# Kernel tuning notes

Measured on AMD Instinct MI355X. Metric: run time of the kernel, lower is better.

Reference implementation:

```python
import jax, jax.numpy as jnp
import numpy as np

N = 50000      # nodes
E = 800000     # edges (avg degree 16)
D = 128        # embed_dim
H = 8          # nhead
HD = D // H    # head dim = 16


def setup_inputs() -> dict:
    key = jax.random.key(0)
    ks = jax.random.split(key, 6)
    s = 1.0 / np.sqrt(D)  # ~xavier scale for square matrices
    return {
        "feats": jax.random.normal(ks[0], (N, D), jnp.float32),
        "edge_index": jax.random.randint(ks[1], (E, 2), 0, N, dtype=jnp.int64),
        "Wq": jax.random.normal(ks[2], (D, D), jnp.float32) * s,
        "bq": jnp.zeros((D,), jnp.float32),
        "Wk": jax.random.normal(ks[3], (D, D), jnp.float32) * s,
        "bk": jnp.zeros((D,), jnp.float32),
        "Wv": jax.random.normal(ks[4], (D, D), jnp.float32) * s,
        "bv": jnp.zeros((D,), jnp.float32),
        "Wo": jax.random.normal(ks[5], (D, D), jnp.float32) * s,
        "bo": jnp.zeros((D,), jnp.float32),
    }


def reference(feats, edge_index, Wq, bq, Wk, bk, Wv, bv, Wo, bo):
    # Projections (nn.Linear: x @ W.T + b), split into heads: [N, H, HD]
    q = (feats @ Wq.T + bq).reshape(N, H, HD)
    k = (feats @ Wk.T + bk).reshape(N, H, HD)
    v = (feats @ Wv.T + bv).reshape(N, H, HD)

    r = edge_index[:, 0]  # source nodes
    c = edge_index[:, 1]  # destination nodes (softmax / aggregation groups)

    # Per-edge, per-head dot-product scores: [E, H]
    scores = jnp.einsum('ehd,ehd->eh', q[c], k[r]) / np.sqrt(HD)

    # Custom scatter-softmax: src_max clamped to min 0; extra exp(-src_max) in denom
    smax = jnp.maximum(jax.ops.segment_max(scores, c, num_segments=N), 0.0)  # [N, H]
    ex = jnp.exp(scores - smax[c])                                           # [E, H]
    denom = jax.ops.segment_sum(ex, c, num_segments=N)                       # [N, H]
    attn = ex / (denom + jnp.exp(-smax))[c]                                  # [E, H]

    # Weighted V per edge, scatter-mean to destination nodes
    out_e = attn[:, :, None] * v[r]                      # [E, H, HD]
    agg = jax.ops.segment_sum(out_e, c, num_segments=N)  # [N, H, HD]
    cnt = jax.ops.segment_sum(jnp.ones((E,), jnp.float32), c, num_segments=N)
    agg = agg / jnp.maximum(cnt, 1.0)[:, None, None]

    return agg.reshape(N, D) @ Wo.T + bo
```

## Files before the change

### kernel.cpp

```cpp
#include <hip/hip_runtime.h>
#include <hip/hip_bf16.h>

#define N_NODES 50000
#define N_EDGES 800000
#define DIM 128
#define NHEAD 8
#define HDIM 16
#define ELL_PAD 64
#define ELL_SLICES 391
#define ELL_BLOCKS (8 * ELL_SLICES)
#define ROWTILES 3125
#define OUT_WAVES (ROWTILES * 2)
#define OUT_GRID ((OUT_WAVES + 3) / 4)

#define Q_OFF      0ull
#define KV_OFF     12800000ull
#define AGG_OFF    38400000ull
#define ELL_OFF    51200000ull
#define CNT_OFF    64000000ull
#define WBF_OFF    64200192ull
#define BIAS_OFF   64331264ull

typedef __attribute__((ext_vector_type(8))) short short8;
typedef __attribute__((ext_vector_type(4))) float floatx4;

__device__ inline float bflo2f(unsigned u) { return __uint_as_float(u << 16); }
__device__ inline float bfhi2f(unsigned u) { return __uint_as_float(u & 0xffff0000u); }
__device__ inline unsigned short f2bf(float f) {
    unsigned u = __float_as_uint(f);
    return (unsigned short)((u + 0x7fffu + ((u >> 16) & 1u)) >> 16);
}

__device__ inline void detect_flags(const void* feats, const void* edge,
                                    int& isbf, int& is32) {
    const unsigned short* f = (const unsigned short*)feats;
    const unsigned int* eg = (const unsigned int*)edge;
    int lane = threadIdx.x & 63;
    unsigned e = (f[lane] >> 7) & 0xFF;
    int junk = (e >= 0x90 || (e > 0 && e <= 0x60)) ? 1 : 0;
    unsigned long long jm = __ballot(junk);
    int nz = (lane < 32 && eg[2 * lane + 1] != 0) ? 1 : 0;
    unsigned long long nm = __ballot(nz);
    isbf = (jm == 0ull) ? 1 : 0;
    is32 = (nm != 0ull) ? 1 : 0;
}

__device__ inline void load_edge(const int* edge, int is32, int e, int& r, int& c) {
    if (is32) { int2 p = ((const int2*)edge)[e]; r = p.x; c = p.y; }
    else {
        const long long* p = (const long long*)edge;
        r = (int)p[2 * e]; c = (int)p[2 * e + 1];
    }
    if ((unsigned)r >= N_NODES) r = 0;
    if ((unsigned)c >= N_NODES) c = 0;
}

__device__ inline float ldf(const void* p, int isbf, int i) {
    return isbf ? __bfloat162float(((const __hip_bfloat16*)p)[i])
                : ((const float*)p)[i];
}

__device__ inline short8 ldfrag(const void* base, int isbf, size_t off) {
    if (isbf) return *(const short8*)((const unsigned short*)base + off);
    const float* f = (const float*)base + off;
    float4 f0 = *(const float4*)f;
    float4 f1 = *(const float4*)(f + 4);
    short8 a;
    a[0] = (short)f2bf(f0.x); a[1] = (short)f2bf(f0.y);
    a[2] = (short)f2bf(f0.z); a[3] = (short)f2bf(f0.w);
    a[4] = (short)f2bf(f1.x); a[5] = (short)f2bf(f1.y);
    a[6] = (short)f2bf(f1.z); a[7] = (short)f2bf(f1.w);
    return a;
}

__global__ __launch_bounds__(256) void ell_build(const void* feats, const int* edge,
                                                 const void* wq, const void* wk,
                                                 const void* wv, const void* wo,
                                                 const void* bq, const void* bk,
                                                 const void* bv, const void* bo,
                                                 int* cnt, int* ell,
                                                 unsigned short* wbf, float* bias) {
    int isbf, is32; detect_flags(feats, edge, isbf, is32);

    if (blockIdx.x >= ELL_BLOCKS) {
        int b2 = blockIdx.x - ELL_BLOCKS;
        if (b2 == 256) {
            for (int j = threadIdx.x; j < 512; j += 256) {
                int m2 = j >> 7;
                const void* bb = (m2 == 0) ? bq : (m2 == 1) ? bk : (m2 == 2) ? bv : bo;
                bias[j] = ldf(bb, isbf, j & 127);
            }
            return;
        }
        if (isbf) return;
        int idx = b2 * 256 + (int)threadIdx.x;
        int mm = idx >> 14, rem = idx & 16383;
        const void* wsrc = (mm == 0) ? wq : (mm == 1) ? wk : (mm == 2) ? wv : wo;
        wbf[idx] = f2bf(((const float*)wsrc)[rem]);
        return;
    }

    int pid = blockIdx.x & 7, slice = blockIdx.x >> 3;
    int base = slice * 2048 + (int)threadIdx.x;
    #pragma unroll
    for (int j = 0; j < 8; ++j) {
        int e = base + j * 256;
        if (e < N_EDGES) {
            int r, c; load_edge(edge, is32, e, r, c);
            if ((c & 7) == pid) {
                int slot = atomicAdd(cnt + c, 1);
                if (slot < ELL_PAD) ell[c * ELL_PAD + slot] = r;
            }
        }
    }
}

__global__ __launch_bounds__(192) void qkv_mfma(const void* feats_raw, const int* edge,
                                                const void* wq_raw, const void* wk_raw,
                                                const void* wv_raw,
                                                const unsigned short* wbf,
                                                const float* bias,
                                                unsigned short* q_s, unsigned short* kv_s) {
    int isbf, is32; detect_flags(feats_raw, edge, isbf, is32);
    int rowtile = blockIdx.x;
    int m = threadIdx.x >> 6;
    int lane = threadIdx.x & 63;
    int mrow = lane & 15, quad = lane >> 4;
    int arow = rowtile * 16 + mrow;

    short8 a[4];
    #pragma unroll
    for (int kt = 0; kt < 4; ++kt)
        a[kt] = ldfrag(feats_raw, isbf, (size_t)arow * DIM + quad * 8 + kt * 32);

    const void* wraw = (m == 0) ? wq_raw : (m == 1) ? wk_raw : wv_raw;
    const unsigned short* wm = isbf ? (const unsigned short*)wraw : wbf + m * 16384;
    int soff = (m == 2) ? 16 : 0;

    for (int nt = 0; nt < 8; ++nt) {
        float b = bias[m * 128 + nt * 16 + mrow];
        floatx4 acc = {b, b, b, b};
        const unsigned short* wp = wm + (size_t)(nt * 16 + mrow) * DIM + quad * 8;
        #pragma unroll
        for (int kt = 0; kt < 4; ++kt) {
            short8 bf = *(const short8*)(wp + kt * 32);
            acc = __builtin_amdgcn_mfma_f32_16x16x32_bf16(a[kt], bf, acc, 0, 0, 0);
        }
        if (m == 0) {
            #pragma unroll
            for (int r4 = 0; r4 < 4; ++r4) {
                int row = rowtile * 16 + quad * 4 + r4;
                q_s[(size_t)row * DIM + nt * 16 + mrow] = f2bf(acc[r4]);
            }
        } else {
            #pragma unroll
            for (int r4 = 0; r4 < 4; ++r4) {
                int row = rowtile * 16 + quad * 4 + r4;
                kv_s[(size_t)row * 256 + nt * 32 + soff + mrow] = f2bf(acc[r4]);
            }
        }
    }
}

__device__ __forceinline__ float dot16(uint4 ka, uint4 kb, const float* qv) {
    float s = 0.f;
    s += bflo2f(ka.x) * qv[0]  + bfhi2f(ka.x) * qv[1];
    s += bflo2f(ka.y) * qv[2]  + bfhi2f(ka.y) * qv[3];
    s += bflo2f(ka.z) * qv[4]  + bfhi2f(ka.z) * qv[5];
    s += bflo2f(ka.w) * qv[6]  + bfhi2f(ka.w) * qv[7];
    s += bflo2f(kb.x) * qv[8]  + bfhi2f(kb.x) * qv[9];
    s += bflo2f(kb.y) * qv[10] + bfhi2f(kb.y) * qv[11];
    s += bflo2f(kb.z) * qv[12] + bfhi2f(kb.z) * qv[13];
    s += bflo2f(kb.w) * qv[14] + bfhi2f(kb.w) * qv[15];
    return s;
}

__device__ __forceinline__ void acc16(float* acc, float p, uint4 va, uint4 vb) {
    acc[0]  += p * bflo2f(va.x); acc[1]  += p * bfhi2f(va.x);
    acc[2]  += p * bflo2f(va.y); acc[3]  += p * bfhi2f(va.y);
    acc[4]  += p * bflo2f(va.z); acc[5]  += p * bfhi2f(va.z);
    acc[6]  += p * bflo2f(va.w); acc[7]  += p * bfhi2f(va.w);
    acc[8]  += p * bflo2f(vb.x); acc[9]  += p * bfhi2f(vb.x);
    acc[10] += p * bflo2f(vb.y); acc[11] += p * bfhi2f(vb.y);
    acc[12] += p * bflo2f(vb.z); acc[13] += p * bfhi2f(vb.z);
    acc[14] += p * bflo2f(vb.w); acc[15] += p * bfhi2f(vb.w);
}

__global__ __launch_bounds__(256) void node_agg(const int* __restrict__ cnt,
                                                const int* __restrict__ ell,
                                                const unsigned short* __restrict__ q_s,
                                                const uint4* __restrict__ kvpack,
                                                uint4* __restrict__ agg_bf) {
    int node = (blockIdx.x * 256 + threadIdx.x) >> 6;
    int lane = threadIdx.x & 63;
    if (node >= N_NODES) return;
    int e = lane >> 3, h = lane & 7;

    const uint4* qp = (const uint4*)(q_s + (size_t)node * DIM + h * HDIM);
    uint4 q0 = qp[0], q1 = qp[1];
    float qv[16];
    qv[0]  = bflo2f(q0.x); qv[1]  = bfhi2f(q0.x);
    qv[2]  = bflo2f(q0.y); qv[3]  = bfhi2f(q0.y);
    qv[4]  = bflo2f(q0.z); qv[5]  = bfhi2f(q0.z);
    qv[6]  = bflo2f(q0.w); qv[7]  = bfhi2f(q0.w);
    qv[8]  = bflo2f(q1.x); qv[9]  = bfhi2f(q1.x);
    qv[10] = bflo2f(q1.y); qv[11] = bfhi2f(q1.y);
    qv[12] = bflo2f(q1.z); qv[13] = bfhi2f(q1.z);
    qv[14] = bflo2f(q1.w); qv[15] = bfhi2f(q1.w);

    int degt = cnt[node];
    int deg = degt < ELL_PAD ? degt : ELL_PAD;
    float l = 0.f;
    float acc[16];
    #pragma unroll
    for (int i = 0; i < 16; ++i) acc[i] = 0.f;

    const int* erow = ell + node * ELL_PAD;
    for (int i0 = 0; i0 < deg; i0 += 32) {
        bool second = (deg - i0) > 16;

        int i1 = i0 + e, i2 = i0 + 8 + e;
        bool ok1 = i1 < deg, ok2 = i2 < deg;
        int r1 = ok1 ? erow[i1] : 0;
        int r2 = ok2 ? erow[i2] : 0;
        const uint4* kp1 = kvpack + (size_t)r1 * 32 + h * 4;
        const uint4* kp2 = kvpack + (size_t)r2 * 32 + h * 4;
        uint4 ka1 = kp1[0], kb1 = kp1[1], va1 = kp1[2], vb1 = kp1[3];
        uint4 ka2 = kp2[0], kb2 = kp2[1], va2 = kp2[2], vb2 = kp2[3];

        if (second) {
            int i3 = i0 + 16 + e, i4 = i0 + 24 + e;
            bool ok3 = i3 < deg, ok4 = i4 < deg;
            int r3 = ok3 ? erow[i3] : 0;
            int r4 = ok4 ? erow[i4] : 0;
            const uint4* kp3 = kvpack + (size_t)r3 * 32 + h * 4;
            const uint4* kp4 = kvpack + (size_t)r4 * 32 + h * 4;
            uint4 ka3 = kp3[0], kb3 = kp3[1], va3 = kp3[2], vb3 = kp3[3];
            uint4 ka4 = kp4[0], kb4 = kp4[1], va4 = kp4[2], vb4 = kp4[3];

            float s1 = dot16(ka1, kb1, qv);
            float p1 = ok1 ? __expf(s1 * 0.25f) : 0.f;
            l += p1; acc16(acc, p1, va1, vb1);

            float s2 = dot16(ka2, kb2, qv);
            float p2 = ok2 ? __expf(s2 * 0.25f) : 0.f;
            l += p2; acc16(acc, p2, va2, vb2);

            float s3 = dot16(ka3, kb3, qv);
            float p3 = ok3 ? __expf(s3 * 0.25f) : 0.f;
            l += p3; acc16(acc, p3, va3, vb3);

            float s4 = dot16(ka4, kb4, qv);
            float p4 = ok4 ? __expf(s4 * 0.25f) : 0.f;
            l += p4; acc16(acc, p4, va4, vb4);
        } else {
            float s1 = dot16(ka1, kb1, qv);
            float p1 = ok1 ? __expf(s1 * 0.25f) : 0.f;
            l += p1; acc16(acc, p1, va1, vb1);

            float s2 = dot16(ka2, kb2, qv);
            float p2 = ok2 ? __expf(s2 * 0.25f) : 0.f;
            l += p2; acc16(acc, p2, va2, vb2);
        }
    }

    #pragma unroll
    for (int m = 8; m < 64; m <<= 1) {
        l += __shfl_xor(l, m);
        #pragma unroll
        for (int i = 0; i < 16; ++i) acc[i] += __shfl_xor(acc[i], m);
    }

    float inv = 1.0f / ((1.0f + l) * (float)(degt > 0 ? degt : 1));
    if (e == 0) {
        unsigned o[8];
        #pragma unroll
        for (int i = 0; i < 8; ++i)
            o[i] = (unsigned)f2bf(acc[2 * i] * inv) | ((unsigned)f2bf(acc[2 * i + 1] * inv) << 16);
        uint4* op = agg_bf + (size_t)node * 16 + h * 2;
        op[0] = make_uint4(o[0], o[1], o[2], o[3]);
        op[1] = make_uint4(o[4], o[5], o[6], o[7]);
    }
}

__global__ __launch_bounds__(256) void out_mfma(const unsigned short* agg_bf,
                                                const void* feats, const int* edge,
                                                const void* wo_raw,
                                                const unsigned short* wbf,
                                                const float* bias, void* out) {
    int isbf, is32; detect_flags(feats, edge, isbf, is32);
    const unsigned short* W = isbf ? (const unsigned short*)wo_raw : wbf + 3 * 16384;
    int w = blockIdx.x * 4 + (threadIdx.x >> 6);
    if (w >= OUT_WAVES) return;
    int rowtile = w >> 1;
    int nthalf = w & 1;
    int lane = threadIdx.x & 63;
    int mrow = lane & 15, quad = lane >> 4;
    int arow = rowtile * 16 + mrow;

    short8 a[4];
    const unsigned short* ap = agg_bf + (size_t)arow * DIM + quad * 8;
    #pragma unroll
    for (int kt = 0; kt < 4; ++kt) a[kt] = *(const short8*)(ap + kt * 32);

    for (int nt = nthalf * 4; nt < nthalf * 4 + 4; ++nt) {
        float b = bias[3 * 128 + nt * 16 + mrow];
        floatx4 acc = {b, b, b, b};
        const unsigned short* wp = W + (size_t)(nt * 16 + mrow) * DIM + quad * 8;
        #pragma unroll
        for (int kt = 0; kt < 4; ++kt) {
            short8 bf = *(const short8*)(wp + kt * 32);
            acc = __builtin_amdgcn_mfma_f32_16x16x32_bf16(a[kt], bf, acc, 0, 0, 0);
        }
        if (isbf) {
            #pragma unroll
            for (int r4 = 0; r4 < 4; ++r4) {
                int row = rowtile * 16 + quad * 4 + r4;
                ((unsigned short*)out)[(size_t)row * DIM + nt * 16 + mrow] = f2bf(acc[r4]);
            }
        } else {
            #pragma unroll
            for (int r4 = 0; r4 < 4; ++r4) {
                int row = rowtile * 16 + quad * 4 + r4;
                ((float*)out)[(size_t)row * DIM + nt * 16 + mrow] = acc[r4];
            }
        }
    }
}

extern "C" void kernel_launch(void* const* d_in, const int* in_sizes, int n_in,
                              void* d_out, int out_size, void* d_ws, size_t ws_size,
                              hipStream_t stream) {
    const void* feats = d_in[0];
    const int*  edge  = (const int*)d_in[1];
    const void* Wq = d_in[2]; const void* bq = d_in[3];
    const void* Wk = d_in[4]; const void* bk = d_in[5];
    const void* Wv = d_in[6]; const void* bv = d_in[7];
    const void* Wo = d_in[8]; const void* bo = d_in[9];

    char* ws = (char*)d_ws;
    unsigned short* q_s  = (unsigned short*)(ws + Q_OFF);
    unsigned short* kv_s = (unsigned short*)(ws + KV_OFF);
    unsigned short* aggb = (unsigned short*)(ws + AGG_OFF);
    int* ell             = (int*)(ws + ELL_OFF);
    int* cnt             = (int*)(ws + CNT_OFF);
    unsigned short* wbf  = (unsigned short*)(ws + WBF_OFF);
    float* bias          = (float*)(ws + BIAS_OFF);

    hipMemsetAsync(ws + CNT_OFF, 0, N_NODES * 4, stream);

    ell_build<<<ELL_BLOCKS + 257, 256, 0, stream>>>(feats, edge, Wq, Wk, Wv, Wo,
                                                    bq, bk, bv, bo, cnt, ell,
                                                    wbf, bias);

    qkv_mfma<<<ROWTILES, 192, 0, stream>>>(feats, edge, Wq, Wk, Wv, wbf, bias,
                                           q_s, kv_s);

    node_agg<<<(N_NODES * 64 + 255) / 256, 256, 0, stream>>>(cnt, ell, q_s,
                                                             (const uint4*)(ws + KV_OFF),
                                                             (uint4*)aggb);

    out_mfma<<<OUT_GRID, 256, 0, stream>>>(aggb, feats, edge, Wo, wbf, bias, d_out);
}
```

Before: 261.9 us.

## Store Q/KV head-major and map node_agg blocks per head with lanes over edges

The QKV projection now writes Q and packed K/V in a head-major layout ([head][node][16/32]) instead of node-major. node_agg is restructured so each block handles one head for 32 nodes: each wave covers 8 nodes, and the 8 lanes of each node stride over its edges. The loop runs until every node in the wave is done, and the cross-lane reduction now spans only 8 lanes. The aim is a smaller per-head gather working set and less register and unroll overhead. The trade-off is that each edge gather becomes a scattered 64-byte access rather than part of a contiguous 512-byte row read by the whole wave.

```diff
diff --git a/kernel.cpp b/kernel.cpp
--- a/kernel.cpp
+++ b/kernel.cpp
@@ -12,6 +12,8 @@
 #define ROWTILES 3125
 #define OUT_WAVES (ROWTILES * 2)
 #define OUT_GRID ((OUT_WAVES + 3) / 4)
+#define AGG_GROUPS 1563
+#define AGG_GRID (AGG_GROUPS * 8)
 
 #define Q_OFF      0ull
 #define KV_OFF     12800000ull
@@ -150,13 +152,13 @@
             #pragma unroll
             for (int r4 = 0; r4 < 4; ++r4) {
                 int row = rowtile * 16 + quad * 4 + r4;
-                q_s[(size_t)row * DIM + nt * 16 + mrow] = f2bf(acc[r4]);
+                q_s[((size_t)nt * N_NODES + row) * 16 + mrow] = f2bf(acc[r4]);
             }
         } else {
             #pragma unroll
             for (int r4 = 0; r4 < 4; ++r4) {
                 int row = rowtile * 16 + quad * 4 + r4;
-                kv_s[(size_t)row * 256 + nt * 32 + soff + mrow] = f2bf(acc[r4]);
+                kv_s[((size_t)nt * N_NODES + row) * 32 + soff + mrow] = f2bf(acc[r4]);
             }
         }
     }
@@ -191,12 +193,17 @@
                                                 const unsigned short* __restrict__ q_s,
                                                 const uint4* __restrict__ kvpack,
                                                 uint4* __restrict__ agg_bf) {
-    int node = (blockIdx.x * 256 + threadIdx.x) >> 6;
+    int h = blockIdx.x & 7;
+    int grp = blockIdx.x >> 3;
+    int w = threadIdx.x >> 6;
     int lane = threadIdx.x & 63;
-    if (node >= N_NODES) return;
-    int e = lane >> 3, h = lane & 7;
-
-    const uint4* qp = (const uint4*)(q_s + (size_t)node * DIM + h * HDIM);
+    int nl = lane >> 3, e = lane & 7;
+    int base = grp * 32 + w * 8;
+    if (base >= N_NODES) return;
+    int node = base + nl;
+
+    const uint4* qp = (const uint4*)((const unsigned short*)q_s
+                                     + ((size_t)h * N_NODES + node) * 16);
     uint4 q0 = qp[0], q1 = qp[1];
     float qv[16];
     qv[0]  = bflo2f(q0.x); qv[1]  = bfhi2f(q0.x);
@@ -216,56 +223,22 @@
     for (int i = 0; i < 16; ++i) acc[i] = 0.f;
 
     const int* erow = ell + node * ELL_PAD;
-    for (int i0 = 0; i0 < deg; i0 += 32) {
-        bool second = (deg - i0) > 16;
-
-        int i1 = i0 + e, i2 = i0 + 8 + e;
-        bool ok1 = i1 < deg, ok2 = i2 < deg;
-        int r1 = ok1 ? erow[i1] : 0;
-        int r2 = ok2 ? erow[i2] : 0;
-        const uint4* kp1 = kvpack + (size_t)r1 * 32 + h * 4;
-        const uint4* kp2 = kvpack + (size_t)r2 * 32 + h * 4;
-        uint4 ka1 = kp1[0], kb1 = kp1[1], va1 = kp1[2], vb1 = kp1[3];
-        uint4 ka2 = kp2[0], kb2 = kp2[1], va2 = kp2[2], vb2 = kp2[3];
-
-        if (second) {
-            int i3 = i0 + 16 + e, i4 = i0 + 24 + e;
-            bool ok3 = i3 < deg, ok4 = i4 < deg;
-            int r3 = ok3 ? erow[i3] : 0;
-            int r4 = ok4 ? erow[i4] : 0;
-            const uint4* kp3 = kvpack + (size_t)r3 * 32 + h * 4;
-            const uint4* kp4 = kvpack + (size_t)r4 * 32 + h * 4;
-            uint4 ka3 = kp3[0], kb3 = kp3[1], va3 = kp3[2], vb3 = kp3[3];
-            uint4 ka4 = kp4[0], kb4 = kp4[1], va4 = kp4[2], vb4 = kp4[3];
-
-            float s1 = dot16(ka1, kb1, qv);
-            float p1 = ok1 ? __expf(s1 * 0.25f) : 0.f;
-            l += p1; acc16(acc, p1, va1, vb1);
-
-            float s2 = dot16(ka2, kb2, qv);
-            float p2 = ok2 ? __expf(s2 * 0.25f) : 0.f;
-            l += p2; acc16(acc, p2, va2, vb2);
-
-            float s3 = dot16(ka3, kb3, qv);
-            float p3 = ok3 ? __expf(s3 * 0.25f) : 0.f;
-            l += p3; acc16(acc, p3, va3, vb3);
-
-            float s4 = dot16(ka4, kb4, qv);
-            float p4 = ok4 ? __expf(s4 * 0.25f) : 0.f;
-            l += p4; acc16(acc, p4, va4, vb4);
-        } else {
-            float s1 = dot16(ka1, kb1, qv);
-            float p1 = ok1 ? __expf(s1 * 0.25f) : 0.f;
-            l += p1; acc16(acc, p1, va1, vb1);
-
-            float s2 = dot16(ka2, kb2, qv);
-            float p2 = ok2 ? __expf(s2 * 0.25f) : 0.f;
-            l += p2; acc16(acc, p2, va2, vb2);
-        }
-    }
-
-    #pragma unroll
-    for (int m = 8; m < 64; m <<= 1) {
+    const uint4* kvh = kvpack + (size_t)h * N_NODES * 4;
+
+    for (int i0 = 0; __any(i0 < deg); i0 += 8) {
+        int i = i0 + e;
+        bool ok = i < deg;
+        int r = ok ? erow[i] : 0;
+        const uint4* kp = kvh + (size_t)r * 4;
+        uint4 ka = kp[0], kb = kp[1], va = kp[2], vb = kp[3];
+        float s = dot16(ka, kb, qv);
+        float p = ok ? __expf(s * 0.25f) : 0.f;
+        l += p;
+        acc16(acc, p, va, vb);
+    }
+
+    #pragma unroll
+    for (int m = 1; m < 8; m <<= 1) {
         l += __shfl_xor(l, m);
         #pragma unroll
         for (int i = 0; i < 16; ++i) acc[i] += __shfl_xor(acc[i], m);
@@ -356,9 +329,9 @@
     qkv_mfma<<<ROWTILES, 192, 0, stream>>>(feats, edge, Wq, Wk, Wv, wbf, bias,
                                            q_s, kv_s);
 
-    node_agg<<<(N_NODES * 64 + 255) / 256, 256, 0, stream>>>(cnt, ell, q_s,
-                                                             (const uint4*)(ws + KV_OFF),
-                                                             (uint4*)aggb);
+    node_agg<<<AGG_GRID, 256, 0, stream>>>(cnt, ell, q_s,
+                                           (const uint4*)(ws + KV_OFF),
+                                           (uint4*)aggb);
 
     out_mfma<<<OUT_GRID, 256, 0, stream>>>(aggb, feats, edge, Wo, wbf, bias, d_out);
 }
```

Result: no change. 262.0 us (+0.0%).
